# Optimization experiments

Hardware: AMD Instinct MI355X
Metric: run time of the kernel (lower is better)

The kernel has to match this reference:

```python
import jax, jax.numpy as jnp
import numpy as np

EPS = 1e-5
NUM_GROUPS = 16


def _deform_conv(x, offset, mask, weight):
    """Modulated deformable conv v2, 3x3, stride 1, pad 1, no bias.
    x: [B,C,H,W], offset: [B,18,H,W] (y,x interleaved per kernel point),
    mask: [B,9,H,W], weight: [O,C,3,3].
    """
    B, C, H, W = x.shape
    O = weight.shape[0]
    K = 9
    off = offset.reshape(B, K, 2, H, W)
    dy, dx = off[:, :, 0], off[:, :, 1]  # [B,K,H,W]
    # base sampling grid: output pixel + kernel tap offset (pad=1 -> taps -1..1)
    ky, kx = jnp.meshgrid(jnp.arange(3), jnp.arange(3), indexing='ij')
    ky = (ky.reshape(K) - 1).astype(x.dtype)
    kx = (kx.reshape(K) - 1).astype(x.dtype)
    iy = jnp.arange(H, dtype=x.dtype)[:, None]
    ix = jnp.arange(W, dtype=x.dtype)[None, :]
    py = iy[None, None] + ky[None, :, None, None] + dy  # [B,K,H,W]
    px = ix[None, None] + kx[None, :, None, None] + dx

    y0 = jnp.floor(py)
    x0 = jnp.floor(px)
    wy = py - y0  # grad flows to offsets via these weights
    wx = px - x0

    xf = x.reshape(B, C, H * W)

    def gather(yc, xc, w):
        # yc,xc,w: [B,K,H,W] float; returns weighted samples [B,C,K,H,W]
        valid = (yc >= 0) & (yc <= H - 1) & (xc >= 0) & (xc <= W - 1)
        yi = jnp.clip(yc, 0, H - 1).astype(jnp.int32)
        xi = jnp.clip(xc, 0, W - 1).astype(jnp.int32)
        idx = (yi * W + xi).reshape(B, K * H * W)
        g = jax.vmap(lambda xb, ib: xb[:, ib])(xf, idx)  # [B,C,K*H*W]
        g = g.reshape(B, C, K, H, W)
        wv = (w * valid.astype(x.dtype))[:, None]  # [B,1,K,H,W]
        return g * wv

    val = gather(y0, x0, (1 - wy) * (1 - wx))
    val = val + gather(y0, x0 + 1, (1 - wy) * wx)
    val = val + gather(y0 + 1, x0, wy * (1 - wx))
    val = val + gather(y0 + 1, x0 + 1, wy * wx)

    val = val * mask[:, None]  # modulation: [B,C,K,H,W] * [B,1,K,H,W]
    w = weight.reshape(O, C, K)
    return jnp.einsum('bckhw,ock->bohw', val, w)


def _group_norm(y, gamma, beta):
    B, O, H, W = y.shape
    g = y.reshape(B, NUM_GROUPS, O // NUM_GROUPS, H, W)
    mean = g.mean(axis=(2, 3, 4), keepdims=True)
    var = ((g - mean) ** 2).mean(axis=(2, 3, 4), keepdims=True)
    g = (g - mean) * jax.lax.rsqrt(var + EPS)
    y = g.reshape(B, O, H, W)
    return y * gamma[None, :, None, None] + beta[None, :, None, None]


def setup_inputs() -> dict:
    key = jax.random.key(0)
    k1, k2, k3, k4 = jax.random.split(key, 4)
    B, C, O, H, W = 8, 256, 256, 64, 64
    x = jax.random.normal(k1, (B, C, H, W), jnp.float32)
    offset = jax.random.normal(k2, (B, 18, H, W), jnp.float32)
    mask = jax.random.uniform(k3, (B, 9, H, W), jnp.float32)
    weight = jax.random.normal(k4, (O, C, 3, 3), jnp.float32) * 0.02
    gamma = jnp.ones((O,), jnp.float32)
    beta = jnp.zeros((O,), jnp.float32)
    return {"x": x, "offset": offset, "mask": mask, "weight": weight,
            "gamma": gamma, "beta": beta}


def reference(x, offset, mask, weight, gamma, beta):
    y = _deform_conv(x, offset, mask, weight)
    return _group_norm(y, gamma, beta)
```

## Files before the change

### kernel.cpp

```cpp
#include <hip/hip_runtime.h>
#include <hip/hip_fp16.h>
#include <math.h>

#define BB 8
#define CC 256
#define OO 256
#define HH 64
#define WW 64
#define KK 9
#define HWSZ 4096
#define CKSZ 2304
#define NG 16
#define OPG 16
#define EPSV 1e-5f

typedef _Float16 f16;
typedef f16 f16x8 __attribute__((ext_vector_type(8)));
typedef float f32x4 __attribute__((ext_vector_type(4)));

#define XH_ELEMS ((size_t)BB*HWSZ*CC)
#define WH_ELEMS ((size_t)OO*CKSZ)
#define CV_ELEMS ((size_t)BB*OO*HWSZ)
#define PSUM_FLOATS ((size_t)512*32)

__device__ __forceinline__ void gload_lds16(const void* g, void* l) {
  __builtin_amdgcn_global_load_lds(
      (const __attribute__((address_space(1))) void*)g,
      (__attribute__((address_space(3))) void*)l, 16, 0, 0);
}

__global__ __launch_bounds__(256) void x_transpose_k(
    const float* __restrict__ x, __half* __restrict__ xh)
{
  int blk = blockIdx.x;
  int b = blk >> 8; int rem = blk & 255;
  int c0 = (rem >> 6) * 64; int hw0 = (rem & 63) * 64;
  __shared__ float st[64][65];
  int t = threadIdx.x;
  #pragma unroll
  for (int i = 0; i < 16; ++i) {
    int idx = t + i*256; int c = idx >> 6, w = idx & 63;
    st[c][w] = x[((size_t)(b*CC + c0 + c))*HWSZ + hw0 + w];
  }
  __syncthreads();
  #pragma unroll
  for (int i = 0; i < 8; ++i) {
    int idx = t + i*256; int r = idx >> 5, cp = idx & 31;
    __half2 v = __floats2half2_rn(st[cp*2][r], st[cp*2+1][r]);
    *(__half2*)&xh[((size_t)(b*HWSZ) + hw0 + r)*CC + c0 + cp*2] = v;
  }
}

__global__ __launch_bounds__(256) void w_reorder_k(
    const float* __restrict__ w, __half* __restrict__ wh)
{
  int i = blockIdx.x*256 + threadIdx.x;
  int o = i / CKSZ; int kp = i - o*CKSZ;
  int kk = kp >> 8, c = kp & 255;
  wh[i] = __float2half(w[o*CKSZ + c*KK + kk]);
}

template<int F16OUT>
__global__ __launch_bounds__(512, 4) void dcn_mfma_k(
    const float* __restrict__ off, const float* __restrict__ msk,
    const __half* __restrict__ xh, const __half* __restrict__ wh,
    float* __restrict__ out32, __half* __restrict__ conv16,
    float* __restrict__ psum)
{
  __shared__ __half sWl[OO*64];
  __shared__ __half sVl[2][64*64];
  __shared__ uint   sTapO[KK][64][4];
  __shared__ __half sTapW[KK][64][4];
  __shared__ float  sRed[8][4][2];

  const int t = threadIdx.x;
  const int b = blockIdx.x & 7;
  const int h = blockIdx.x >> 3;

  const int lane = t & 63, wid = t >> 6;
  const int wm = wid & 3, wn = wid >> 2;
  const int lr = lane & 15, lh = lane >> 4;
  const int gp = t >> 3, goct = t & 7;

  for (int s = t; s < KK*64; s += 512) {
    int k = s >> 6, p = s & 63;
    float dy = off[(((b*18) + 2*k    )*HH + h)*WW + p];
    float dx = off[(((b*18) + 2*k + 1)*HH + h)*WW + p];
    float m  = msk[(((b*KK) + k)*HH + h)*WW + p];
    float py = (float)(h + (k/3) - 1) + dy;
    float px = (float)(p + (k%3) - 1) + dx;
    float y0f = floorf(py), x0f = floorf(px);
    float wy = py - y0f, wx = px - x0f;
    int y0 = (int)y0f, x0 = (int)x0f;
    #pragma unroll
    for (int tap = 0; tap < 4; ++tap) {
      int yy = y0 + (tap >> 1), xx = x0 + (tap & 1);
      bool v = (yy >= 0) & (yy < HH) & (xx >= 0) & (xx < WW);
      float bw = ((tap >> 1) ? wy : 1.f - wy) * ((tap & 1) ? wx : 1.f - wx);
      float wgt = v ? bw * m : 0.f;
      int cy = min(max(yy, 0), HH-1), cx = min(max(xx, 0), WW-1);
      sTapO[k][p][tap] = (uint)((cy*WW + cx) * (CC*2));
      sTapW[k][p][tap] = __float2half(wgt);
    }
  }
  __syncthreads();

  f32x4 acc[4][2];
  #pragma unroll
  for (int mi = 0; mi < 4; ++mi)
    #pragma unroll
    for (int ni = 0; ni < 2; ++ni) acc[mi][ni] = (f32x4){0.f,0.f,0.f,0.f};

  const char* xbase = (const char*)xh + (size_t)b * (HWSZ*CC*2);

  uint4 tO = *(const uint4*)&sTapO[0][gp][0];
  union { uint2 u; __half hh[4]; } tW;
  tW.u = *(const uint2*)&sTapW[0][gp][0];

  auto gload_sw = [&](int k, int c0) {
    #pragma unroll
    for (int i = 0; i < 4; ++i) {
      int idx = i*512 + t;
      int o = idx >> 3, s = idx & 7;
      const __half* g = wh + (size_t)o*CKSZ + k*256 + c0 + ((s ^ (o & 7)) << 3);
      char* ldsbase = (char*)sWl + (size_t)(i*512 + (t & ~63))*16;
      gload_lds16(g, ldsbase);
    }
  };

  gload_sw(0, 0);
  {
    const char* cb = xbase + goct*16;
    uint4 r0 = *(const uint4*)(cb + tO.x);
    uint4 r1 = *(const uint4*)(cb + tO.y);
    uint4 r2 = *(const uint4*)(cb + tO.z);
    uint4 r3 = *(const uint4*)(cb + tO.w);
    __half2 w0 = __half2half2(tW.hh[0]), w1 = __half2half2(tW.hh[1]);
    __half2 w2 = __half2half2(tW.hh[2]), w3 = __half2half2(tW.hh[3]);
    const __half2* t0 = (const __half2*)&r0; const __half2* t1 = (const __half2*)&r1;
    const __half2* t2 = (const __half2*)&r2; const __half2* t3 = (const __half2*)&r3;
    __half2 o_[4];
    #pragma unroll
    for (int r = 0; r < 4; ++r)
      o_[r] = __hfma2(w0, t0[r], __hfma2(w1, t1[r],
              __hfma2(w2, t2[r], __hmul2(w3, t3[r]))));
    *(uint4*)&sVl[0][gp*64 + ((goct ^ (gp & 7)) << 3)] = *(uint4*)o_;
  }

  int cur = 0;
  for (int cc = 0; cc < 36; ++cc) {
    const int k  = cc >> 2;
    __syncthreads();

    f16x8 areg[2][4];
    #pragma unroll
    for (int ks = 0; ks < 2; ++ks)
      #pragma unroll
      for (int mi = 0; mi < 4; ++mi) {
        int r = wm*64 + mi*16 + lr;
        areg[ks][mi] = *(const f16x8*)&sWl[r*64 + (((ks*4 + lh) ^ (r & 7)) << 3)];
      }
    __syncthreads();

    uint4 g0, g1, g2, g3;
    bool pf = (cc + 1 < 36);
    int kn = (cc+1) >> 2, c0n = ((cc+1) & 3) << 6;
    if (pf) {
      gload_sw(kn, c0n);
      if (kn != k) {
        tO = *(const uint4*)&sTapO[kn][gp][0];
        tW.u = *(const uint2*)&sTapW[kn][gp][0];
      }
      const char* cb = xbase + (size_t)(c0n*2) + goct*16;
      g0 = *(const uint4*)(cb + tO.x);
      g1 = *(const uint4*)(cb + tO.y);
      g2 = *(const uint4*)(cb + tO.z);
      g3 = *(const uint4*)(cb + tO.w);
    }

    #pragma unroll
    for (int ks = 0; ks < 2; ++ks) {
      f16x8 brg[2];
      #pragma unroll
      for (int ni = 0; ni < 2; ++ni) {
        int r = wn*32 + ni*16 + lr;
        brg[ni] = *(const f16x8*)&sVl[cur][r*64 + (((ks*4 + lh) ^ (r & 7)) << 3)];
      }
      #pragma unroll
      for (int mi = 0; mi < 4; ++mi)
        #pragma unroll
        for (int ni = 0; ni < 2; ++ni)
          acc[mi][ni] = __builtin_amdgcn_mfma_f32_16x16x32_f16(
              areg[ks][mi], brg[ni], acc[mi][ni], 0, 0, 0);
    }

    if (pf) {
      __half2 w0 = __half2half2(tW.hh[0]), w1 = __half2half2(tW.hh[1]);
      __half2 w2 = __half2half2(tW.hh[2]), w3 = __half2half2(tW.hh[3]);
      const __half2* t0 = (const __half2*)&g0; const __half2* t1 = (const __half2*)&g1;
      const __half2* t2 = (const __half2*)&g2; const __half2* t3 = (const __half2*)&g3;
      __half2 o_[4];
      #pragma unroll
      for (int r = 0; r < 4; ++r)
        o_[r] = __hfma2(w0, t0[r], __hfma2(w1, t1[r],
                __hfma2(w2, t2[r], __hmul2(w3, t3[r]))));
      *(uint4*)&sVl[cur ^ 1][gp*64 + ((goct ^ (gp & 7)) << 3)] = *(uint4*)o_;
      cur ^= 1;
    }
  }

  #pragma unroll
  for (int mi = 0; mi < 4; ++mi) {
    #pragma unroll
    for (int ni = 0; ni < 2; ++ni) {
      int ob = wm*64 + mi*16 + lh*4;
      int pp = wn*32 + ni*16 + lr;
      #pragma unroll
      for (int j = 0; j < 4; ++j) {
        size_t idx = ((size_t)(b*OO + ob + j))*HWSZ + h*WW + pp;
        if (F16OUT) conv16[idx] = __float2half(acc[mi][ni][j]);
        else        out32[idx] = acc[mi][ni][j];
      }
    }
  }

  if (F16OUT) {
    #pragma unroll
    for (int mi = 0; mi < 4; ++mi) {
      float s1 = 0.f, s2 = 0.f;
      #pragma unroll
      for (int ni = 0; ni < 2; ++ni)
        #pragma unroll
        for (int j = 0; j < 4; ++j) {
          float v = acc[mi][ni][j];
          s1 += v; s2 += v*v;
        }
      #pragma unroll
      for (int d = 32; d > 0; d >>= 1) {
        s1 += __shfl_xor(s1, d);
        s2 += __shfl_xor(s2, d);
      }
      if (lane == 0) { sRed[wid][mi][0] = s1; sRed[wid][mi][1] = s2; }
    }
    __syncthreads();
    if (t < 16) {
      int gwm = t >> 2, gmi = t & 3;
      float s1 = sRed[gwm][gmi][0] + sRed[4 + gwm][gmi][0];
      float s2 = sRed[gwm][gmi][1] + sRed[4 + gwm][gmi][1];
      psum[(size_t)blockIdx.x*32 + t*2]     = s1;
      psum[(size_t)blockIdx.x*32 + t*2 + 1] = s2;
    }
  }
}

__global__ __launch_bounds__(256) void gn_norm2_k(
    const __half* __restrict__ conv16, const float* __restrict__ psum,
    const float* __restrict__ gamma, const float* __restrict__ beta,
    float* __restrict__ out)
{
  int bid = blockIdx.x;
  int bo = bid >> 1;
  int b = bo >> 8, o = bo & 255;
  int g = o >> 4;
  float s1 = 0.f, s2 = 0.f;
  for (int hbl = 0; hbl < 64; ++hbl) {
    s1 += psum[(size_t)(hbl*8 + b)*32 + g*2];
    s2 += psum[(size_t)(hbl*8 + b)*32 + g*2 + 1];
  }
  const float invN = 1.f / (float)(OPG*HWSZ);
  float mean = s1 * invN;
  float var  = s2 * invN - mean*mean;
  float inv = rsqrtf(var + EPSV);
  float sc = gamma[o]*inv;
  float sh = beta[o] - mean*sc;

  size_t e0 = ((size_t)(b*OO + o))*HWSZ + (size_t)(bid & 1)*2048
            + (size_t)threadIdx.x*8;
  uint4 u = *(const uint4*)(conv16 + e0);
  const __half2* hh = (const __half2*)&u;
  float r[8];
  #pragma unroll
  for (int j = 0; j < 4; ++j) {
    float2 f = __half22float2(hh[j]);
    r[2*j] = f.x; r[2*j+1] = f.y;
  }
  *(float4*)&out[e0]     = make_float4(r[0]*sc+sh, r[1]*sc+sh, r[2]*sc+sh, r[3]*sc+sh);
  *(float4*)&out[e0 + 4] = make_float4(r[4]*sc+sh, r[5]*sc+sh, r[6]*sc+sh, r[7]*sc+sh);
}

__global__ __launch_bounds__(1024) void gn_stats_k(
    const float* __restrict__ out, float* __restrict__ stats)
{
  int bg = blockIdx.x;
  const float4* p = (const float4*)(out + (size_t)bg*OPG*HWSZ);
  const int n4 = OPG*HWSZ/4;
  float s1 = 0.f, s2 = 0.f;
  for (int i = threadIdx.x; i < n4; i += 1024) {
    float4 v = p[i];
    s1 += v.x + v.y + v.z + v.w;
    s2 += v.x*v.x + v.y*v.y + v.z*v.z + v.w*v.w;
  }
  #pragma unroll
  for (int o2 = 32; o2 > 0; o2 >>= 1) {
    s1 += __shfl_down(s1, o2);
    s2 += __shfl_down(s2, o2);
  }
  __shared__ float r1[16], r2[16];
  int wd = threadIdx.x >> 6, lane = threadIdx.x & 63;
  if (lane == 0) { r1[wd] = s1; r2[wd] = s2; }
  __syncthreads();
  if (threadIdx.x == 0) {
    float t1 = 0.f, t2 = 0.f;
    #pragma unroll
    for (int i = 0; i < 16; i++) { t1 += r1[i]; t2 += r2[i]; }
    const float invN = 1.f / (float)(OPG*HWSZ);
    float mean = t1 * invN;
    float var  = t2 * invN - mean*mean;
    stats[bg*2]   = mean;
    stats[bg*2+1] = var;
  }
}

__global__ __launch_bounds__(256) void gn_norm_k(
    float* __restrict__ out, const float* __restrict__ stats,
    const float* __restrict__ gamma, const float* __restrict__ beta)
{
  size_t i = (size_t)blockIdx.x*256 + threadIdx.x;
  const size_t n4 = (size_t)BB*OO*HWSZ/4;
  if (i >= n4) return;
  size_t base = i*4;
  int bo = (int)(base / HWSZ);
  int b = bo / OO, o = bo - b*OO;
  int g = o >> 4;
  float mean = stats[(b*NG+g)*2], var = stats[(b*NG+g)*2+1];
  float inv = rsqrtf(var + EPSV);
  float sc = gamma[o]*inv;
  float sh = beta[o] - mean*sc;
  float4 v = *(float4*)&out[base];
  v.x = v.x*sc + sh; v.y = v.y*sc + sh;
  v.z = v.z*sc + sh; v.w = v.w*sc + sh;
  *(float4*)&out[base] = v;
}

extern "C" void kernel_launch(void* const* d_in, const int* in_sizes, int n_in,
                              void* d_out, int out_size, void* d_ws, size_t ws_size,
                              hipStream_t stream) {
  const float* x      = (const float*)d_in[0];
  const float* offset = (const float*)d_in[1];
  const float* mask   = (const float*)d_in[2];
  const float* weight = (const float*)d_in[3];
  const float* gamma  = (const float*)d_in[4];
  const float* beta   = (const float*)d_in[5];
  float* out = (float*)d_out;

  __half* xh   = (__half*)d_ws;
  __half* wh   = xh + XH_ELEMS;
  __half* cv   = wh + WH_ELEMS;
  float* psum  = (float*)(cv + CV_ELEMS);

  const size_t need = (XH_ELEMS + WH_ELEMS + CV_ELEMS)*2 + PSUM_FLOATS*4 + 1024;

  x_transpose_k<<<BB*4*64, 256, 0, stream>>>(x, xh);
  w_reorder_k<<<(int)(WH_ELEMS/256), 256, 0, stream>>>(weight, wh);

  if (ws_size >= need) {
    dcn_mfma_k<1><<<512, 512, 0, stream>>>(offset, mask, xh, wh,
                                           (float*)nullptr, cv, psum);
    gn_norm2_k<<<4096, 256, 0, stream>>>(cv, psum, gamma, beta, out);
  } else {
    float* stats = (float*)(wh + WH_ELEMS);
    dcn_mfma_k<0><<<512, 512, 0, stream>>>(offset, mask, xh, wh,
                                           out, (__half*)nullptr, (float*)nullptr);
    gn_stats_k<<<BB*NG, 1024, 0, stream>>>(out, stats);
    gn_norm_k<<<(int)((size_t)BB*OO*HWSZ/4 + 255)/256, 256, 0, stream>>>(
        out, stats, gamma, beta);
  }
}
```

Before: 92.56 us.

## Use 4-wave blocks with 64x64 per-warp output tiles in deformable conv

```diff
diff --git a/kernel.cpp b/kernel.cpp
--- a/kernel.cpp
+++ b/kernel.cpp
@@ -61,7 +61,7 @@
 }
 
 template<int F16OUT>
-__global__ __launch_bounds__(512, 4) void dcn_mfma_k(
+__global__ __launch_bounds__(256, 2) void dcn_mfma_k(
     const float* __restrict__ off, const float* __restrict__ msk,
     const __half* __restrict__ xh, const __half* __restrict__ wh,
     float* __restrict__ out32, __half* __restrict__ conv16,
@@ -71,18 +71,17 @@
   __shared__ __half sVl[2][64*64];
   __shared__ uint   sTapO[KK][64][4];
   __shared__ __half sTapW[KK][64][4];
-  __shared__ float  sRed[8][4][2];
+  __shared__ float  sRed[4][4][2];
 
   const int t = threadIdx.x;
   const int b = blockIdx.x & 7;
   const int h = blockIdx.x >> 3;
 
   const int lane = t & 63, wid = t >> 6;
-  const int wm = wid & 3, wn = wid >> 2;
   const int lr = lane & 15, lh = lane >> 4;
-  const int gp = t >> 3, goct = t & 7;
-
-  for (int s = t; s < KK*64; s += 512) {
+  const int gp = t >> 2, gq = t & 3;
+
+  for (int s = t; s < KK*64; s += 256) {
     int k = s >> 6, p = s & 63;
     float dy = off[(((b*18) + 2*k    )*HH + h)*WW + p];
     float dx = off[(((b*18) + 2*k + 1)*HH + h)*WW + p];
@@ -105,11 +104,11 @@
   }
   __syncthreads();
 
-  f32x4 acc[4][2];
+  f32x4 acc[4][4];
   #pragma unroll
   for (int mi = 0; mi < 4; ++mi)
     #pragma unroll
-    for (int ni = 0; ni < 2; ++ni) acc[mi][ni] = (f32x4){0.f,0.f,0.f,0.f};
+    for (int ni = 0; ni < 4; ++ni) acc[mi][ni] = (f32x4){0.f,0.f,0.f,0.f};
 
   const char* xbase = (const char*)xh + (size_t)b * (HWSZ*CC*2);
 
@@ -119,37 +118,41 @@
 
   auto gload_sw = [&](int k, int c0) {
     #pragma unroll
-    for (int i = 0; i < 4; ++i) {
-      int idx = i*512 + t;
+    for (int i = 0; i < 8; ++i) {
+      int idx = i*256 + t;
       int o = idx >> 3, s = idx & 7;
       const __half* g = wh + (size_t)o*CKSZ + k*256 + c0 + ((s ^ (o & 7)) << 3);
-      char* ldsbase = (char*)sWl + (size_t)(i*512 + (t & ~63))*16;
+      char* ldsbase = (char*)sWl + (size_t)(i*256 + (t & ~63))*16;
       gload_lds16(g, ldsbase);
     }
   };
 
   gload_sw(0, 0);
   {
-    const char* cb = xbase + goct*16;
-    uint4 r0 = *(const uint4*)(cb + tO.x);
-    uint4 r1 = *(const uint4*)(cb + tO.y);
-    uint4 r2 = *(const uint4*)(cb + tO.z);
-    uint4 r3 = *(const uint4*)(cb + tO.w);
     __half2 w0 = __half2half2(tW.hh[0]), w1 = __half2half2(tW.hh[1]);
     __half2 w2 = __half2half2(tW.hh[2]), w3 = __half2half2(tW.hh[3]);
-    const __half2* t0 = (const __half2*)&r0; const __half2* t1 = (const __half2*)&r1;
-    const __half2* t2 = (const __half2*)&r2; const __half2* t3 = (const __half2*)&r3;
-    __half2 o_[4];
-    #pragma unroll
-    for (int r = 0; r < 4; ++r)
-      o_[r] = __hfma2(w0, t0[r], __hfma2(w1, t1[r],
-              __hfma2(w2, t2[r], __hmul2(w3, t3[r]))));
-    *(uint4*)&sVl[0][gp*64 + ((goct ^ (gp & 7)) << 3)] = *(uint4*)o_;
+    #pragma unroll
+    for (int oi = 0; oi < 2; ++oi) {
+      int oct = gq + oi*4;
+      const char* cb = xbase + oct*16;
+      uint4 r0 = *(const uint4*)(cb + tO.x);
+      uint4 r1 = *(const uint4*)(cb + tO.y);
+      uint4 r2 = *(const uint4*)(cb + tO.z);
+      uint4 r3 = *(const uint4*)(cb + tO.w);
+      const __half2* t0 = (const __half2*)&r0; const __half2* t1 = (const __half2*)&r1;
+      const __half2* t2 = (const __half2*)&r2; const __half2* t3 = (const __half2*)&r3;
+      __half2 o_[4];
+      #pragma unroll
+      for (int r = 0; r < 4; ++r)
+        o_[r] = __hfma2(w0, t0[r], __hfma2(w1, t1[r],
+                __hfma2(w2, t2[r], __hmul2(w3, t3[r]))));
+      *(uint4*)&sVl[0][gp*64 + ((oct ^ (gp & 7)) << 3)] = *(uint4*)o_;
+    }
   }
 
   int cur = 0;
   for (int cc = 0; cc < 36; ++cc) {
-    const int k  = cc >> 2;
+    const int k = cc >> 2;
     __syncthreads();
 
     f16x8 areg[2][4];
@@ -157,12 +160,12 @@
     for (int ks = 0; ks < 2; ++ks)
       #pragma unroll
       for (int mi = 0; mi < 4; ++mi) {
-        int r = wm*64 + mi*16 + lr;
+        int r = wid*64 + mi*16 + lr;
         areg[ks][mi] = *(const f16x8*)&sWl[r*64 + (((ks*4 + lh) ^ (r & 7)) << 3)];
       }
     __syncthreads();
 
-    uint4 g0, g1, g2, g3;
+    uint4 ga0, ga1, ga2, ga3, gb0, gb1, gb2, gb3;
     bool pf = (cc + 1 < 36);
     int kn = (cc+1) >> 2, c0n = ((cc+1) & 3) << 6;
     if (pf) {
@@ -171,25 +174,29 @@
         tO = *(const uint4*)&sTapO[kn][gp][0];
         tW.u = *(const uint2*)&sTapW[kn][gp][0];
       }
-      const char* cb = xbase + (size_t)(c0n*2) + goct*16;
-      g0 = *(const uint4*)(cb + tO.x);
-      g1 = *(const uint4*)(cb + tO.y);
-      g2 = *(const uint4*)(cb + tO.z);
-      g3 = *(const uint4*)(cb + tO.w);
+      const char* cb = xbase + (size_t)(c0n*2) + gq*16;
+      ga0 = *(const uint4*)(cb + tO.x);
+      ga1 = *(const uint4*)(cb + tO.y);
+      ga2 = *(const uint4*)(cb + tO.z);
+      ga3 = *(const uint4*)(cb + tO.w);
+      gb0 = *(const uint4*)(cb + tO.x + 64);
+      gb1 = *(const uint4*)(cb + tO.y + 64);
+      gb2 = *(const uint4*)(cb + tO.z + 64);
+      gb3 = *(const uint4*)(cb + tO.w + 64);
     }
 
     #pragma unroll
     for (int ks = 0; ks < 2; ++ks) {
-      f16x8 brg[2];
-      #pragma unroll
-      for (int ni = 0; ni < 2; ++ni) {
-        int r = wn*32 + ni*16 + lr;
+      f16x8 brg[4];
+      #pragma unroll
+      for (int ni = 0; ni < 4; ++ni) {
+        int r = ni*16 + lr;
         brg[ni] = *(const f16x8*)&sVl[cur][r*64 + (((ks*4 + lh) ^ (r & 7)) << 3)];
       }
       #pragma unroll
       for (int mi = 0; mi < 4; ++mi)
         #pragma unroll
-        for (int ni = 0; ni < 2; ++ni)
+        for (int ni = 0; ni < 4; ++ni)
           acc[mi][ni] = __builtin_amdgcn_mfma_f32_16x16x32_f16(
               areg[ks][mi], brg[ni], acc[mi][ni], 0, 0, 0);
     }
@@ -197,14 +204,26 @@
     if (pf) {
       __half2 w0 = __half2half2(tW.hh[0]), w1 = __half2half2(tW.hh[1]);
       __half2 w2 = __half2half2(tW.hh[2]), w3 = __half2half2(tW.hh[3]);
-      const __half2* t0 = (const __half2*)&g0; const __half2* t1 = (const __half2*)&g1;
-      const __half2* t2 = (const __half2*)&g2; const __half2* t3 = (const __half2*)&g3;
-      __half2 o_[4];
-      #pragma unroll
-      for (int r = 0; r < 4; ++r)
-        o_[r] = __hfma2(w0, t0[r], __hfma2(w1, t1[r],
-                __hfma2(w2, t2[r], __hmul2(w3, t3[r]))));
-      *(uint4*)&sVl[cur ^ 1][gp*64 + ((goct ^ (gp & 7)) << 3)] = *(uint4*)o_;
+      {
+        const __half2* t0 = (const __half2*)&ga0; const __half2* t1 = (const __half2*)&ga1;
+        const __half2* t2 = (const __half2*)&ga2; const __half2* t3 = (const __half2*)&ga3;
+        __half2 o_[4];
+        #pragma unroll
+        for (int r = 0; r < 4; ++r)
+          o_[r] = __hfma2(w0, t0[r], __hfma2(w1, t1[r],
+                  __hfma2(w2, t2[r], __hmul2(w3, t3[r]))));
+        *(uint4*)&sVl[cur ^ 1][gp*64 + ((gq ^ (gp & 7)) << 3)] = *(uint4*)o_;
+      }
+      {
+        const __half2* t0 = (const __half2*)&gb0; const __half2* t1 = (const __half2*)&gb1;
+        const __half2* t2 = (const __half2*)&gb2; const __half2* t3 = (const __half2*)&gb3;
+        __half2 o_[4];
+        #pragma unroll
+        for (int r = 0; r < 4; ++r)
+          o_[r] = __hfma2(w0, t0[r], __hfma2(w1, t1[r],
+                  __hfma2(w2, t2[r], __hmul2(w3, t3[r]))));
+        *(uint4*)&sVl[cur ^ 1][gp*64 + (((gq + 4) ^ (gp & 7)) << 3)] = *(uint4*)o_;
+      }
       cur ^= 1;
     }
   }
@@ -212,9 +231,9 @@
   #pragma unroll
   for (int mi = 0; mi < 4; ++mi) {
     #pragma unroll
-    for (int ni = 0; ni < 2; ++ni) {
-      int ob = wm*64 + mi*16 + lh*4;
-      int pp = wn*32 + ni*16 + lr;
+    for (int ni = 0; ni < 4; ++ni) {
+      int ob = wid*64 + mi*16 + lh*4;
+      int pp = ni*16 + lr;
       #pragma unroll
       for (int j = 0; j < 4; ++j) {
         size_t idx = ((size_t)(b*OO + ob + j))*HWSZ + h*WW + pp;
@@ -229,7 +248,7 @@
     for (int mi = 0; mi < 4; ++mi) {
       float s1 = 0.f, s2 = 0.f;
       #pragma unroll
-      for (int ni = 0; ni < 2; ++ni)
+      for (int ni = 0; ni < 4; ++ni)
         #pragma unroll
         for (int j = 0; j < 4; ++j) {
           float v = acc[mi][ni][j];
@@ -244,11 +263,8 @@
     }
     __syncthreads();
     if (t < 16) {
-      int gwm = t >> 2, gmi = t & 3;
-      float s1 = sRed[gwm][gmi][0] + sRed[4 + gwm][gmi][0];
-      float s2 = sRed[gwm][gmi][1] + sRed[4 + gwm][gmi][1];
-      psum[(size_t)blockIdx.x*32 + t*2]     = s1;
-      psum[(size_t)blockIdx.x*32 + t*2 + 1] = s2;
+      psum[(size_t)blockIdx.x*32 + t*2]     = sRed[t >> 2][t & 3][0];
+      psum[(size_t)blockIdx.x*32 + t*2 + 1] = sRed[t >> 2][t & 3][1];
     }
   }
 }
@@ -364,12 +380,12 @@
   w_reorder_k<<<(int)(WH_ELEMS/256), 256, 0, stream>>>(weight, wh);
 
   if (ws_size >= need) {
-    dcn_mfma_k<1><<<512, 512, 0, stream>>>(offset, mask, xh, wh,
+    dcn_mfma_k<1><<<512, 256, 0, stream>>>(offset, mask, xh, wh,
                                            (float*)nullptr, cv, psum);
     gn_norm2_k<<<4096, 256, 0, stream>>>(cv, psum, gamma, beta, out);
   } else {
     float* stats = (float*)(wh + WH_ELEMS);
-    dcn_mfma_k<0><<<512, 512, 0, stream>>>(offset, mask, xh, wh,
+    dcn_mfma_k<0><<<512, 256, 0, stream>>>(offset, mask, xh, wh,
                                            out, (__half*)nullptr, (float*)nullptr);
     gn_stats_k<<<BB*NG, 1024, 0, stream>>>(out, stats);
     gn_norm_k<<<(int)((size_t)BB*OO*HWSZ/4 + 255)/256, 256, 0, stream>>>(
```

New measurement: 93.41 us. About the same (+0.9%).
